# Kernel tuning notes

Measured on AMD Instinct MI355X. Metric: run time of the kernel, lower is better.

## Reference

```python
import jax, jax.numpy as jnp
import numpy as np

V = 128
L = 128
N = 4096

_ALPHA = "abcdefghijklmnopqrstuvwxyz"
TOKENS = (list("+-*/^()=") + [f"temp_{a}" for a in _ALPHA]
          + [str(d) for d in range(10)] + [f"w{i}" for i in range(84)])
assert len(TOKENS) == V
IDX = {t: i for i, t in enumerate(TOKENS)}
TEMPS = [f"temp_{a}" for a in _ALPHA]


def _build_mask_table() -> np.ndarray:
    """mask_table[p, v] = 0 if token v is illegal after prev-token p, else 1.
    Mirrors RuleFilter.single_filter's rho for every possible prev token."""
    M = np.ones((V, V), dtype=np.float32)

    def ban(prev_tokens, banned_tokens):
        cols = [IDX[t] for t in banned_tokens]
        for p in prev_tokens:
            M[IDX[p], cols] = 0.0

    ban(list("+-*/"), list("+-*/)="))          # prev is binary op
    ban(TEMPS, list("(="))                      # prev is temp_* variable
    ban(["="], list("+-*/=)") + TEMPS)         # prev is '='
    ban(["("], list("()+-*/="))                # prev is '('
    ban([")"], list("()") + TEMPS)             # prev is ')'
    ban(["^"], list("+-*/=)"))                 # prev is '^'
    return M


def setup_inputs() -> dict:
    key = jax.random.key(0)
    logits = jax.random.normal(key, (L, N, V), dtype=jnp.float32)
    mask_table = jnp.asarray(_build_mask_table())  # (V, V) rule lookup
    return {"logits": logits, "mask_table": mask_table}


def reference(logits, mask_table):
    """logits: (L, N, V); mask_table: (V, V). Sequential rule masking:
    logits[i] *= mask_table[argmax(filtered logits[i-1])]."""
    first = logits[0]  # row 0 is never filtered

    def step(carry, cur):
        # carry: previously *filtered* logits row (N, V)
        prev_idx = jnp.argmax(carry, axis=-1)          # (N,)
        new = cur * mask_table[prev_idx]               # gather + multiply
        return new, new

    _, rest = jax.lax.scan(step, first, logits[1:])
    return jnp.concatenate([first[None], rest], axis=0)
```

## Files before the change

kernel.cpp:

```cpp
#include <hip/hip_runtime.h>
#include <string.h>


constexpr int V = 128;
constexpr int L = 128;
constexpr int N = 4096;

__device__ __forceinline__ float wave_max_dpp(float x) {
    int v = __float_as_int(x);
    const int ninf = __float_as_int(-__builtin_inff());
#define RF_STEP(ctrl)                                                          \
    {                                                                          \
        int s = __builtin_amdgcn_update_dpp(ninf, v, ctrl, 0xf, 0xf, false);   \
        v = __float_as_int(fmaxf(__int_as_float(v), __int_as_float(s)));       \
    }
    RF_STEP(0x111)
    RF_STEP(0x112)
    RF_STEP(0x114)
    RF_STEP(0x118)
    RF_STEP(0x142)
    RF_STEP(0x143)
#undef RF_STEP
    return __int_as_float(__builtin_amdgcn_readlane(v, 63));
}

__device__ __forceinline__ int wave_argmax(float2 f) {
    const float bv = wave_max_dpp(fmaxf(f.x, f.y));
    unsigned long long b0 = __ballot(f.x == bv);
    unsigned long long b1 = __ballot(f.y == bv);
    int i0 = __ffsll(b0);
    int i1 = __ffsll(b1);
    int c0 = i0 ? (i0 - 1) * 2 : (1 << 30);
    int c1 = i1 ? (i1 - 1) * 2 + 1 : (1 << 30);
    return min(c0, c1);
}

__device__ __forceinline__ unsigned sel8(const unsigned* t, int j) {
    unsigned a0 = (j & 1) ? t[1] : t[0];
    unsigned a1 = (j & 1) ? t[3] : t[2];
    unsigned a2 = (j & 1) ? t[5] : t[4];
    unsigned a3 = (j & 1) ? t[7] : t[6];
    unsigned b0 = (j & 2) ? a1 : a0;
    unsigned b1 = (j & 2) ? a3 : a2;
    return (j & 4) ? b1 : b0;
}

__global__ __launch_bounds__(256) void rule_filter_kernel(
    const float* __restrict__ logits,
    const float* __restrict__ mask_table,
    float* __restrict__ out)
{
    const int wave = threadIdx.x >> 6;
    const int lane = threadIdx.x & 63;
    const int n    = (blockIdx.x << 2) + wave;

    const size_t base    = (size_t)n * V + (size_t)(lane * 2);
    const size_t rstride = (size_t)N * V;

    unsigned tbl[8];
#pragma unroll 1
    for (int j = 0; j < 8; ++j) {
        unsigned acc = 0;
#pragma unroll
        for (int r = 0; r < 16; ++r) {
            const int p = j * 16 + r;
            float2 mv = *(const float2*)(mask_table + (size_t)p * V + lane * 2);
            acc |= ((mv.x != 0.0f ? 1u : 0u) | (mv.y != 0.0f ? 2u : 0u)) << (2 * r);
        }
        tbl[j] = acc;
    }

    auto ld = [&](int i) -> float2 {
        return *(const float2*)(logits + (size_t)i * rstride + base);
    };
    auto st = [&](int i, float2 v) {
        long long bits;
        memcpy(&bits, &v, 8);
        __builtin_nontemporal_store(bits, (long long*)(out + (size_t)i * rstride + base));
    };

    constexpr int D = 8;
    float2 buf[D];
#pragma unroll
    for (int k = 0; k < D; ++k) buf[k] = ld(k);

    st(0, buf[0]);
    int prev = wave_argmax(buf[0]);

#pragma unroll 8
    for (int i = 1; i < L; ++i) {
        float2 c = buf[i & (D - 1)];
        const int pf = (i + D - 1 < L) ? (i + D - 1) : (L - 1);
        buf[pf & (D - 1)] = ld(pf);

        const unsigned word  = sel8(tbl, prev >> 4);
        const unsigned fbits = (word >> ((prev & 15) * 2)) & 3u;
        float2 f;
        f.x = (fbits & 1u) ? c.x : 0.0f;
        f.y = (fbits & 2u) ? c.y : 0.0f;

        st(i, f);
        prev = wave_argmax(f);
    }
}

extern "C" void kernel_launch(void* const* d_in, const int* in_sizes, int n_in,
                              void* d_out, int out_size, void* d_ws, size_t ws_size,
                              hipStream_t stream) {
    const float* logits     = (const float*)d_in[0];
    const float* mask_table = (const float*)d_in[1];
    float* out              = (float*)d_out;

    dim3 grid(N / 4);
    dim3 block(256);
    rule_filter_kernel<<<grid, block, 0, stream>>>(logits, mask_table, out);
}
```

Baseline: 507.0 us.

## Stage logits rows through per-wave LDS ring with deeper async prefetch

Replaces the 8-deep register prefetch of logits rows with a 16-slot per-wave LDS ring buffer. The ring is filled by global_load_lds direct-to-LDS loads issued 15 rows ahead, with manual s_waitcnt vmcnt throttling. The aim is to hide global load latency on the serial argmax-dependent chain and to free registers, adding a launch-bounds occupancy hint. The hand-chosen vmcnt threshold ignores that stores also count toward vmcnt, so the waits are likely more conservative than intended. This adds 32KB of LDS per block.

```diff
diff --git a/kernel.cpp b/kernel.cpp
--- a/kernel.cpp
+++ b/kernel.cpp
@@ -5,6 +5,9 @@
 constexpr int V = 128;
 constexpr int L = 128;
 constexpr int N = 4096;
+constexpr int SLOTS = 16;
+constexpr int DIST  = 15;
+constexpr int WAITN = 28;
 
 __device__ __forceinline__ float wave_max_dpp(float x) {
     int v = __float_as_int(x);
@@ -45,17 +48,27 @@
     return (j & 4) ? b1 : b0;
 }
 
-__global__ __launch_bounds__(256) void rule_filter_kernel(
+typedef __attribute__((address_space(1))) const float* gas1_cfp;
+typedef __attribute__((address_space(3))) float*       las3_fp;
+
+__device__ __forceinline__ void stage_word(const float* g, float* l) {
+    __builtin_amdgcn_global_load_lds((gas1_cfp)g, (las3_fp)l, 4, 0, 0);
+}
+
+__global__ __launch_bounds__(256, 4) void rule_filter_kernel(
     const float* __restrict__ logits,
     const float* __restrict__ mask_table,
     float* __restrict__ out)
 {
+    __shared__ float ring[4][SLOTS][V];
+
     const int wave = threadIdx.x >> 6;
     const int lane = threadIdx.x & 63;
     const int n    = (blockIdx.x << 2) + wave;
 
-    const size_t base    = (size_t)n * V + (size_t)(lane * 2);
     const size_t rstride = (size_t)N * V;
+    const float* seq     = logits + (size_t)n * V;
+    const size_t obase   = (size_t)n * V + (size_t)(lane * 2);
 
     unsigned tbl[8];
 #pragma unroll 1
@@ -69,29 +82,32 @@
         }
         tbl[j] = acc;
     }
+    asm volatile("s_waitcnt vmcnt(0)" ::: "memory");
 
-    auto ld = [&](int i) -> float2 {
-        return *(const float2*)(logits + (size_t)i * rstride + base);
-    };
+    float* const my = &ring[wave][0][0];
+
+#pragma unroll 1
+    for (int r = 0; r < SLOTS; ++r) {
+        const float* rp = seq + (size_t)r * rstride;
+        float* lp = my + r * V;
+        stage_word(rp + lane,      lp);
+        stage_word(rp + 64 + lane, lp + 64);
+    }
+
     auto st = [&](int i, float2 v) {
         long long bits;
         memcpy(&bits, &v, 8);
-        __builtin_nontemporal_store(bits, (long long*)(out + (size_t)i * rstride + base));
+        __builtin_nontemporal_store(bits, (long long*)(out + (size_t)i * rstride + obase));
     };
 
-    constexpr int D = 8;
-    float2 buf[D];
-#pragma unroll
-    for (int k = 0; k < D; ++k) buf[k] = ld(k);
+    asm volatile("s_waitcnt vmcnt(" "28" ")" ::: "memory");
+    float2 c0 = *(const float2*)(my + 2 * lane);
+    st(0, c0);
+    int prev = wave_argmax(c0);
 
-    st(0, buf[0]);
-    int prev = wave_argmax(buf[0]);
-
-#pragma unroll 8
     for (int i = 1; i < L; ++i) {
-        float2 c = buf[i & (D - 1)];
-        const int pf = (i + D - 1 < L) ? (i + D - 1) : (L - 1);
-        buf[pf & (D - 1)] = ld(pf);
+        asm volatile("s_waitcnt vmcnt(28)" ::: "memory");
+        float2 c = *(const float2*)(my + (i & (SLOTS - 1)) * V + 2 * lane);
 
         const unsigned word  = sel8(tbl, prev >> 4);
         const unsigned fbits = (word >> ((prev & 15) * 2)) & 3u;
@@ -101,6 +117,12 @@
 
         st(i, f);
         prev = wave_argmax(f);
+
+        const int pf = (i + DIST < L) ? (i + DIST) : (L - 1);
+        const float* rp = seq + (size_t)pf * rstride;
+        float* lp = my + (pf & (SLOTS - 1)) * V;
+        stage_word(rp + lane,      lp);
+        stage_word(rp + 64 + lane, lp + 64);
     }
 }
 
```

Result: faster. 477.1 us (-5.9%).

## Hand-schedule loads and stores with inline asm and exact vmcnt waits

Applied to the files above, without the earlier changes.

Replaces the compiler-scheduled prefetch loop with a fully unrolled template recursion that issues global loads and nontemporal stores through inline asm, using scalar base addresses plus 32-bit lane offsets. Each step waits with a computed vmcnt, so only the needed row's load must be done and stores stay in flight. Prefetch depth goes from 8 to 16 rows, and launch bounds ask for 4 blocks per CU. The aim is to keep more memory requests outstanding and stop the compiler from inserting conservative full waits. The cost is higher register pressure and fragile asm that depends on exact counting of outstanding operations.

```diff
diff --git a/kernel.cpp b/kernel.cpp
--- a/kernel.cpp
+++ b/kernel.cpp
@@ -1,10 +1,13 @@
 #include <hip/hip_runtime.h>
-#include <string.h>
 
 
 constexpr int V = 128;
 constexpr int L = 128;
 constexpr int N = 4096;
+constexpr int D = 16;
+constexpr unsigned ROWB = (unsigned)N * V * 4;
+
+typedef __attribute__((ext_vector_type(2))) float f32x2;
 
 __device__ __forceinline__ float wave_max_dpp(float x) {
     int v = __float_as_int(x);
@@ -24,7 +27,7 @@
     return __int_as_float(__builtin_amdgcn_readlane(v, 63));
 }
 
-__device__ __forceinline__ int wave_argmax(float2 f) {
+__device__ __forceinline__ int wave_argmax(f32x2 f) {
     const float bv = wave_max_dpp(fmaxf(f.x, f.y));
     unsigned long long b0 = __ballot(f.x == bv);
     unsigned long long b1 = __ballot(f.y == bv);
@@ -45,7 +48,66 @@
     return (j & 4) ? b1 : b0;
 }
 
-__global__ __launch_bounds__(256) void rule_filter_kernel(
+__device__ __forceinline__ unsigned long long uniform_u64(const void* p) {
+    unsigned long long x = (unsigned long long)p;
+    unsigned lo = __builtin_amdgcn_readfirstlane((unsigned)x);
+    unsigned hi = __builtin_amdgcn_readfirstlane((unsigned)(x >> 32));
+    return ((unsigned long long)hi << 32) | lo;
+}
+
+template <int I>
+struct Step {
+    static __device__ __forceinline__ void run(f32x2* ring, f32x2* fbuf,
+                                               const unsigned* tbl, int& prev,
+                                               unsigned long long lbase,
+                                               unsigned long long obase,
+                                               unsigned laneoff) {
+        constexpr int NW = (I <= 15) ? (15 + I) : ((I <= L - D - 1) ? 30 : (15 + (L - 1 - I)));
+        constexpr int s  = I & (D - 1);
+
+        asm volatile("s_waitcnt vmcnt(%c2)"
+                     : "+v"(ring[s])
+                     : "v"(fbuf[s]), "i"(NW));
+
+        f32x2 c = ring[s];
+        f32x2 f;
+        if (I == 0) {
+            f = c;
+        } else {
+            const unsigned word  = sel8(tbl, prev >> 4);
+            const unsigned fbits = (word >> ((prev & 15) * 2)) & 3u;
+            f.x = (fbits & 1u) ? c.x : 0.0f;
+            f.y = (fbits & 2u) ? c.y : 0.0f;
+        }
+        fbuf[s] = f;
+
+        {
+            unsigned voff = (unsigned)I * ROWB + laneoff;
+            asm volatile("global_store_dwordx2 %0, %1, %2 nt"
+                         :
+                         : "v"(voff), "v"(fbuf[s]), "s"(obase));
+        }
+
+        prev = wave_argmax(f);
+
+        if constexpr (I + D < L) {
+            unsigned voff = (unsigned)(I + D) * ROWB + laneoff;
+            asm volatile("global_load_dwordx2 %0, %1, %2"
+                         : "=&v"(ring[s])
+                         : "v"(voff), "s"(lbase));
+        }
+
+        Step<I + 1>::run(ring, fbuf, tbl, prev, lbase, obase, laneoff);
+    }
+};
+template <>
+struct Step<L> {
+    static __device__ __forceinline__ void run(f32x2*, f32x2*, const unsigned*,
+                                               int&, unsigned long long,
+                                               unsigned long long, unsigned) {}
+};
+
+__global__ __launch_bounds__(256, 4) void rule_filter_kernel(
     const float* __restrict__ logits,
     const float* __restrict__ mask_table,
     float* __restrict__ out)
@@ -54,8 +116,9 @@
     const int lane = threadIdx.x & 63;
     const int n    = (blockIdx.x << 2) + wave;
 
-    const size_t base    = (size_t)n * V + (size_t)(lane * 2);
-    const size_t rstride = (size_t)N * V;
+    const unsigned long long lbase = uniform_u64(logits + (size_t)n * V);
+    const unsigned long long obase = uniform_u64(out    + (size_t)n * V);
+    const unsigned laneoff = (unsigned)lane * 8;
 
     unsigned tbl[8];
 #pragma unroll 1
@@ -69,39 +132,23 @@
         }
         tbl[j] = acc;
     }
+    asm volatile("s_waitcnt vmcnt(0)" ::: "memory");
 
-    auto ld = [&](int i) -> float2 {
-        return *(const float2*)(logits + (size_t)i * rstride + base);
-    };
-    auto st = [&](int i, float2 v) {
-        long long bits;
-        memcpy(&bits, &v, 8);
-        __builtin_nontemporal_store(bits, (long long*)(out + (size_t)i * rstride + base));
-    };
+    f32x2 ring[D];
+    f32x2 fbuf[D];
+#pragma unroll
+    for (int r = 0; r < D; ++r) { fbuf[r].x = 0.0f; fbuf[r].y = 0.0f; }
 
-    constexpr int D = 8;
-    float2 buf[D];
 #pragma unroll
-    for (int k = 0; k < D; ++k) buf[k] = ld(k);
+    for (int r = 0; r < D; ++r) {
+        unsigned voff = (unsigned)r * ROWB + laneoff;
+        asm volatile("global_load_dwordx2 %0, %1, %2"
+                     : "=&v"(ring[r])
+                     : "v"(voff), "s"(lbase));
+    }
 
-    st(0, buf[0]);
-    int prev = wave_argmax(buf[0]);
-
-#pragma unroll 8
-    for (int i = 1; i < L; ++i) {
-        float2 c = buf[i & (D - 1)];
-        const int pf = (i + D - 1 < L) ? (i + D - 1) : (L - 1);
-        buf[pf & (D - 1)] = ld(pf);
-
-        const unsigned word  = sel8(tbl, prev >> 4);
-        const unsigned fbits = (word >> ((prev & 15) * 2)) & 3u;
-        float2 f;
-        f.x = (fbits & 1u) ? c.x : 0.0f;
-        f.y = (fbits & 2u) ? c.y : 0.0f;
-
-        st(i, f);
-        prev = wave_argmax(f);
-    }
+    int prev = 0;
+    Step<0>::run(ring, fbuf, tbl, prev, lbase, obase, laneoff);
 }
 
 extern "C" void kernel_launch(void* const* d_in, const int* in_sizes, int n_in,
```

New measurement: 450.1 us. -11.2%, faster.
